# Kernel optimization log

Measured on AMD Instinct MI355X. Metric: run time of the kernel, lower is better.

Reference implementation:

```python
import jax, jax.numpy as jnp
import numpy as np

ALPHABET = 26

def _shift(position, S):
    if position == 0:
        return jnp.zeros(S, dtype=jnp.int32)
    elif position == 1:
        return jnp.arange(S, dtype=jnp.int32) % ALPHABET
    elif position == 2:
        return jnp.arange(S, dtype=jnp.int32) // 26 + 1 % 26  # faithful to torch precedence: +1
    elif position == 3:
        return jnp.arange(S, dtype=jnp.int32) // 676 + 1 % 26
    raise ValueError('Invalid rotor position')


def setup_inputs() -> dict:
    key = jax.random.key(0)
    k1, k2 = jax.random.split(key)
    B, S = 128, 8192
    signalInput = jax.random.normal(k1, (B, S, ALPHABET), dtype=jnp.float32)
    # xavier_normal_ on a 26x26 matrix: std = sqrt(2/(26+26))
    std = float(np.sqrt(2.0 / (ALPHABET + ALPHABET)))
    rotor = jax.random.normal(k2, (ALPHABET, ALPHABET), dtype=jnp.float32) * std
    return {"signalInput": signalInput, "rotor": rotor}


def reference(signalInput, rotor):
    position = 1
    B, S, _ = signalInput.shape
    # L2-normalize rotor rows (torch.norm(dim=1, keepdim=True))
    rn = rotor / jnp.linalg.norm(rotor, axis=1, keepdims=True)  # [26,26]
    shift = _shift(position, S)                                  # [S]
    # one_hot((i + shift[s]) % 26) @ rn  ==  gather rn rows
    idx = (jnp.arange(ALPHABET, dtype=jnp.int32)[None, :] + shift[:, None]) % ALPHABET  # [S,26]
    M = rn[idx]                                                  # [S,26,26]
    # per-token 1x26 @ 26x26 bmm, batch-independent rotation matrix
    out = jnp.einsum('bsi,sij->bsj', signalInput, M)             # [B,S,26]
    return jax.nn.softmax(out, axis=2)
```

## Files before the change

### kernel.cpp

```cpp
#include <hip/hip_runtime.h>
#include <math.h>

#define ALPHA 26
#define TPB 256
#define ROWF 26
#define WAVEF (64 * ROWF)
#define BUFF (4 * WAVEF)
#define NBLK 768

typedef __attribute__((ext_vector_type(8))) short short8;
typedef __attribute__((ext_vector_type(4))) float float4v;
typedef __attribute__((address_space(3))) float lds_f;
typedef const __attribute__((address_space(1))) float glb_f;

__device__ __forceinline__ unsigned short f2bf(float f) {
    unsigned u = __builtin_bit_cast(unsigned, f);
    u += 0x7FFFu + ((u >> 16) & 1u);
    return (unsigned short)(u >> 16);
}

__global__ void rotor_norm_kernel(const float* __restrict__ rotor,
                                  unsigned short* __restrict__ rnbT) {
    __shared__ float inv[32];
    const int t = threadIdx.x;
    if (t < 32) {
        float s = 0.f;
        if (t < ALPHA) {
            #pragma unroll
            for (int j = 0; j < ALPHA; ++j) {
                float v = rotor[t * ALPHA + j];
                s += v * v;
            }
            inv[t] = 1.0f / sqrtf(s);
        } else {
            inv[t] = 0.f;
        }
    }
    __syncthreads();
    const int n  = t >> 1;
    const int k0 = (t & 1) * 16;
    #pragma unroll
    for (int kk = 0; kk < 16; ++kk) {
        const int k = k0 + kk;
        float v = (k < ALPHA && n < ALPHA) ? rotor[k * ALPHA + n] * inv[k] : 0.f;
        rnbT[n * 32 + k] = f2bf(v);
    }
}

__global__ __launch_bounds__(TPB, 3) void rotor_main(
        const float* __restrict__ x,
        const unsigned short* __restrict__ rnbT,
        float* __restrict__ out,
        int ntiles) {
    __shared__ float stage[2 * BUFF];

    const int tid  = threadIdx.x;
    const int lane = tid & 63;
    const int wave = tid >> 6;
    const int n15  = lane & 15;
    const int quad = lane >> 4;
    const int waveF = wave * WAVEF;

    short8 bf0 = *(const short8*)(rnbT + n15 * 32 + quad * 8);
    short8 bf1 = *(const short8*)(rnbT + (n15 + 16) * 32 + quad * 8);

    int tile = blockIdx.x;
    if (tile >= ntiles) return;
    const int stride = gridDim.x;

    auto prefetch = [&](int buf, int t) {
        const float* gp = x + (long long)t * (TPB * ALPHA) + waveF;
        lds_f* lp = (lds_f*)&stage[buf * BUFF + waveF];
        #pragma unroll
        for (int it = 0; it < 6; ++it)
            __builtin_amdgcn_global_load_lds((glb_f*)(gp + it * 256 + lane * 4),
                                             lp + it * 256, 16, 0, 0);
        __builtin_amdgcn_global_load_lds((glb_f*)(gp + 1536 + lane), lp + 1536, 4, 0, 0);
        __builtin_amdgcn_global_load_lds((glb_f*)(gp + 1600 + lane), lp + 1600, 4, 0, 0);
    };

    prefetch(0, tile);

    int i = 0;
    for (; tile < ntiles; tile += stride, ++i) {
        if (i == 0) asm volatile("s_waitcnt vmcnt(0)" ::: "memory");
        else        asm volatile("s_waitcnt vmcnt(7)" ::: "memory");

        const int cur = i & 1;
        const int tnext = tile + stride;
        if (tnext < ntiles) prefetch(cur ^ 1, tnext);
        asm volatile("" ::: "memory");

        const int sbase   = cur * BUFF + waveF;
        const int tokBase = tile * TPB + wave * 64;

        float4v accA[4], accB[4];
        #pragma unroll
        for (int m = 0; m < 4; ++m) {
            accA[m] = (float4v){0.f, 0.f, 0.f, 0.f};
            accB[m] = (float4v){0.f, 0.f, 0.f, 0.f};
        }

        #pragma unroll
        for (int m = 0; m < 4; ++m) {
            const int tok = tokBase + m * 16 + n15;
            const int r = (tok & 8191) % 26;
            const int rowOff = sbase + (m * 16 + n15) * ROWF;
            const int k0 = quad * 8;
            int idx0 = k0 - r; if (idx0 < 0) idx0 += 26;

            short8 af;
            #pragma unroll
            for (int j = 0; j < 8; ++j) {
                int idx = idx0 + j; if (idx >= 26) idx -= 26;
                af[j] = (short)f2bf(stage[rowOff + idx]);
            }
            accA[m] = __builtin_amdgcn_mfma_f32_16x16x32_bf16(af, bf0, accA[m], 0, 0, 0);
            accB[m] = __builtin_amdgcn_mfma_f32_16x16x32_bf16(af, bf1, accB[m], 0, 0, 0);
        }

        #pragma unroll
        for (int m = 0; m < 4; ++m) {
            #pragma unroll
            for (int rg = 0; rg < 4; ++rg) {
                const int base = sbase + (m * 16 + quad * 4 + rg) * ROWF;
                stage[base + n15] = accA[m][rg];
                if (n15 < ALPHA - 16)
                    stage[base + 16 + n15] = accB[m][rg];
            }
        }

        const float* myrow = &stage[sbase + lane * ROWF];
        float v[ALPHA];
        #pragma unroll
        for (int j = 0; j < ALPHA; ++j) v[j] = myrow[j];
        float mx = v[0];
        #pragma unroll
        for (int j = 1; j < ALPHA; ++j) mx = fmaxf(mx, v[j]);
        float sum = 0.f;
        #pragma unroll
        for (int j = 0; j < ALPHA; ++j) { v[j] = __expf(v[j] - mx); sum += v[j]; }
        float inv = 1.0f / sum;
        float* wrow = &stage[sbase + lane * ROWF];
        #pragma unroll
        for (int j = 0; j < ALPHA; ++j) wrow[j] = v[j] * inv;

        float* gout = out + (long long)tile * (TPB * ALPHA) + waveF;
        #pragma unroll
        for (int it = 0; it < 6; ++it) {
            float4 d = *(const float4*)&stage[sbase + it * 256 + lane * 4];
            *(float4*)(gout + it * 256 + lane * 4) = d;
        }
        {
            float2 d = *(const float2*)&stage[sbase + 1536 + lane * 2];
            *(float2*)(gout + 1536 + lane * 2) = d;
        }
    }
}

extern "C" void kernel_launch(void* const* d_in, const int* in_sizes, int n_in,
                              void* d_out, int out_size, void* d_ws, size_t ws_size,
                              hipStream_t stream) {
    const float* x     = (const float*)d_in[0];
    const float* rotor = (const float*)d_in[1];
    float* out = (float*)d_out;
    unsigned short* rnbT = (unsigned short*)d_ws;

    rotor_norm_kernel<<<1, 64, 0, stream>>>(rotor, rnbT);

    const int tokens = out_size / ALPHA;
    const int tiles  = tokens / TPB;
    const int grid   = (tiles < NBLK) ? tiles : NBLK;
    rotor_main<<<grid, TPB, 0, stream>>>(x, rnbT, out, tiles);
}
```

Baseline: 198.1 us.

## Compute softmax in MFMA accumulator layout with DPP reductions and store directly

The softmax now runs on the MFMA accumulators in registers. Row max and row sum are reduced across each 16-lane DPP row with row_ror shuffles, and the results go straight to global memory as nontemporal scalar stores. This removes the LDS round trip: the scatter of accumulators, the per-lane 26-float reload, the write-back and the re-read for vectorised stores. The vmcnt wait threshold is raised because the many outstanding stores now share the counter with the prefetch loads. The cost is narrower, strided global stores (16 plus 10 floats per row) in place of coalesced float4 writes, which may hurt store efficiency.

```diff
diff --git a/kernel.cpp b/kernel.cpp
--- a/kernel.cpp
+++ b/kernel.cpp
@@ -17,6 +17,13 @@
     unsigned u = __builtin_bit_cast(unsigned, f);
     u += 0x7FFFu + ((u >> 16) & 1u);
     return (unsigned short)(u >> 16);
+}
+
+template<int CTRL>
+__device__ __forceinline__ float rorf(float v) {
+    int s = __builtin_bit_cast(int, v);
+    int d = __builtin_amdgcn_update_dpp(s, s, CTRL, 0xf, 0xf, false);
+    return __builtin_bit_cast(float, d);
 }
 
 __global__ void rotor_norm_kernel(const float* __restrict__ rotor,
@@ -84,7 +91,7 @@
     int i = 0;
     for (; tile < ntiles; tile += stride, ++i) {
         if (i == 0) asm volatile("s_waitcnt vmcnt(0)" ::: "memory");
-        else        asm volatile("s_waitcnt vmcnt(7)" ::: "memory");
+        else        asm volatile("s_waitcnt vmcnt(16)" ::: "memory");
 
         const int cur = i & 1;
         const int tnext = tile + stride;
@@ -104,10 +111,10 @@
         #pragma unroll
         for (int m = 0; m < 4; ++m) {
             const int tok = tokBase + m * 16 + n15;
-            const int r = (tok & 8191) % 26;
+            const int r_ = (tok & 8191) % 26;
             const int rowOff = sbase + (m * 16 + n15) * ROWF;
             const int k0 = quad * 8;
-            int idx0 = k0 - r; if (idx0 < 0) idx0 += 26;
+            int idx0 = k0 - r_; if (idx0 < 0) idx0 += 26;
 
             short8 af;
             #pragma unroll
@@ -123,37 +130,27 @@
         for (int m = 0; m < 4; ++m) {
             #pragma unroll
             for (int rg = 0; rg < 4; ++rg) {
-                const int base = sbase + (m * 16 + quad * 4 + rg) * ROWF;
-                stage[base + n15] = accA[m][rg];
+                float a = accA[m][rg];
+                float b = accB[m][rg];
+                float mx = fmaxf(a, b);
+                mx = fmaxf(mx, rorf<0x121>(mx));
+                mx = fmaxf(mx, rorf<0x122>(mx));
+                mx = fmaxf(mx, rorf<0x124>(mx));
+                mx = fmaxf(mx, rorf<0x128>(mx));
+                float ea = __expf(a - mx);
+                float eb = (n15 < ALPHA - 16) ? __expf(b - mx) : 0.f;
+                float s = ea + eb;
+                s += rorf<0x121>(s);
+                s += rorf<0x122>(s);
+                s += rorf<0x124>(s);
+                s += rorf<0x128>(s);
+                float inv = 1.0f / s;
+                float* gouts = out +
+                    (long long)(tokBase + m * 16 + quad * 4 + rg) * ALPHA;
+                __builtin_nontemporal_store(ea * inv, gouts + n15);
                 if (n15 < ALPHA - 16)
-                    stage[base + 16 + n15] = accB[m][rg];
+                    __builtin_nontemporal_store(eb * inv, gouts + 16 + n15);
             }
-        }
-
-        const float* myrow = &stage[sbase + lane * ROWF];
-        float v[ALPHA];
-        #pragma unroll
-        for (int j = 0; j < ALPHA; ++j) v[j] = myrow[j];
-        float mx = v[0];
-        #pragma unroll
-        for (int j = 1; j < ALPHA; ++j) mx = fmaxf(mx, v[j]);
-        float sum = 0.f;
-        #pragma unroll
-        for (int j = 0; j < ALPHA; ++j) { v[j] = __expf(v[j] - mx); sum += v[j]; }
-        float inv = 1.0f / sum;
-        float* wrow = &stage[sbase + lane * ROWF];
-        #pragma unroll
-        for (int j = 0; j < ALPHA; ++j) wrow[j] = v[j] * inv;
-
-        float* gout = out + (long long)tile * (TPB * ALPHA) + waveF;
-        #pragma unroll
-        for (int it = 0; it < 6; ++it) {
-            float4 d = *(const float4*)&stage[sbase + it * 256 + lane * 4];
-            *(float4*)(gout + it * 256 + lane * 4) = d;
-        }
-        {
-            float2 d = *(const float2*)&stage[sbase + 1536 + lane * 2];
-            *(float2*)(gout + 1536 + lane * 2) = d;
         }
     }
 }
```

Measured after the change: 246.2 us. 1.24x slower.
